# Kernel optimization log

Measured on AMD Instinct MI355X. Metric: run time of the kernel, lower is better.

Reference implementation:

```python
import jax, jax.numpy as jnp
import numpy as np

B, X_DIM, Y_DIM, HIDDEN = 512, 768, 128, 1024
H2 = HIDDEN // 2


def setup_inputs() -> dict:
    key = jax.random.key(0)
    ks = jax.random.split(key, 10)
    s_in = 1.0 / np.sqrt(X_DIM)
    s_h = 1.0 / np.sqrt(H2)
    return {
        "x_samples": jax.random.normal(ks[0], (B, X_DIM), jnp.float32),
        "y_samples": jax.random.normal(ks[1], (B, Y_DIM), jnp.float32),
        "w1_mu": jax.random.uniform(ks[2], (X_DIM, H2), jnp.float32, -s_in, s_in),
        "b1_mu": jax.random.uniform(ks[3], (H2,), jnp.float32, -s_in, s_in),
        "w2_mu": jax.random.uniform(ks[4], (H2, Y_DIM), jnp.float32, -s_h, s_h),
        "b2_mu": jax.random.uniform(ks[5], (Y_DIM,), jnp.float32, -s_h, s_h),
        "w1_lv": jax.random.uniform(ks[6], (X_DIM, H2), jnp.float32, -s_in, s_in),
        "b1_lv": jax.random.uniform(ks[7], (H2,), jnp.float32, -s_in, s_in),
        "w2_lv": jax.random.uniform(ks[8], (H2, Y_DIM), jnp.float32, -s_h, s_h),
        "b2_lv": jax.random.uniform(ks[9], (Y_DIM,), jnp.float32, -s_h, s_h),
    }


def reference(x_samples, y_samples, w1_mu, b1_mu, w2_mu, b2_mu,
              w1_lv, b1_lv, w2_lv, b2_lv):
    batch = y_samples.shape[0]
    # p_mu / p_logvar MLP heads
    mu = jax.nn.relu(x_samples @ w1_mu + b1_mu) @ w2_mu + b2_mu          # [B, Y]
    logvar = jnp.tanh(jax.nn.relu(x_samples @ w1_lv + b1_lv) @ w2_lv + b2_lv)  # [B, Y]

    inv_var = jnp.exp(-logvar)
    # positive: diagonal Gaussian log-prob of y_i under p(.|x_i), up to const
    positive = (-0.5 * (mu - y_samples) ** 2 * inv_var - 0.5 * logvar).sum(-1)  # [B]

    # pairwise log-probs: row i = params from x_i, col j = sample y_j
    mu_1 = mu[:, None, :]            # [B, 1, Y]
    lv_1 = logvar[:, None, :]        # [B, 1, Y]
    y_1 = y_samples[None, :, :]      # [1, B, Y]
    all_probs = (-0.5 * (y_1 - mu_1) ** 2 * jnp.exp(-lv_1) - 0.5 * lv_1).sum(-1)  # [B, B]

    # Faithful replication of the torch broadcasting: diag_mask is [B, B, 1],
    # so all_probs + diag_mask broadcasts to [B, B, B], then logsumexp over dim 0.
    diag_mask = (jnp.eye(batch, dtype=all_probs.dtype) * -20.0)[:, :, None]  # [B, B, 1]
    logits = all_probs + diag_mask                                           # [B, B, B]
    negative = jax.scipy.special.logsumexp(logits, axis=0) - jnp.log(batch - 1.0)  # [B, B]

    return (positive - negative).mean()
```

## Files before the change

### kernel.cpp

```cpp
#include <hip/hip_runtime.h>
#include <math.h>

#define BSZ   512
#define XD    768
#define YD    128
#define H2D   512

__global__ __launch_bounds__(256, 2) void layer1_kernel(
    const float* __restrict__ x,
    const float* __restrict__ w1_mu, const float* __restrict__ w1_lv,
    const float* __restrict__ y,
    float* __restrict__ p1,
    double* __restrict__ Sy, double* __restrict__ Sy2,
    double* __restrict__ accum, unsigned int* __restrict__ counter)
{
    __shared__ float As[16][68];
    __shared__ float Bs[16][68];
    const int t = threadIdx.x;

    if (blockIdx.z == 4) {
        const int id = blockIdx.x + 8 * blockIdx.y;
        if (id >= 16) return;
        const int dl = t & 7;
        const int g  = t >> 3;
        const int d  = id * 8 + dl;
        float s = 0.f, s2 = 0.f;
        for (int i = g * 16; i < g * 16 + 16; ++i) {
            const float v = y[i * YD + d];
            s += v; s2 += v * v;
        }
        float* shs  = &As[0][0];
        float* shs2 = &Bs[0][0];
        shs[t] = s; shs2[t] = s2;
        __syncthreads();
        if (t < 8) {
            double S = 0.0, S2 = 0.0;
            #pragma unroll
            for (int gg = 0; gg < 32; ++gg) {
                S += (double)shs[gg * 8 + t]; S2 += (double)shs2[gg * 8 + t];
            }
            Sy[id * 8 + t] = S; Sy2[id * 8 + t] = S2;
        } else if (id == 0 && t == 8)  { accum[0] = 0.0; }
        else if (id == 0 && t == 9)  { accum[1] = 0.0; }
        else if (id == 0 && t == 10) { *counter = 0u; }
        return;
    }

    const int bz     = blockIdx.z;
    const int branch = bz >> 1;
    const int ks     = bz & 1;
    const float* __restrict__ W = branch ? w1_lv : w1_mu;
    float* __restrict__ out = p1 + (size_t)bz * (BSZ * H2D);

    const int m0 = blockIdx.x * 64;
    const int n0 = blockIdx.y * 64;
    const int tx = t & 15;
    const int ty = t >> 4;

    const int am  = t >> 2;
    const int akq = (t & 3) << 2;
    const int bkk = t >> 4;
    const int bnq = (t & 15) << 2;

    const int kbase = ks * 384;
    float acc[4][4] = {};

    float4 a_pref = *(const float4*)&x[(m0 + am) * XD + kbase + akq];
    float4 b_pref = *(const float4*)&W[(kbase + bkk) * H2D + n0 + bnq];

    for (int kt = 0; kt < 384; kt += 16) {
        __syncthreads();
        As[akq + 0][am] = a_pref.x;
        As[akq + 1][am] = a_pref.y;
        As[akq + 2][am] = a_pref.z;
        As[akq + 3][am] = a_pref.w;
        *(float4*)&Bs[bkk][bnq] = b_pref;
        __syncthreads();
        if (kt + 16 < 384) {
            const int kn = kbase + kt + 16;
            a_pref = *(const float4*)&x[(m0 + am) * XD + kn + akq];
            b_pref = *(const float4*)&W[(kn + bkk) * H2D + n0 + bnq];
        }
        #pragma unroll
        for (int k = 0; k < 16; ++k) {
            const float4 av = *(const float4*)&As[k][ty * 4];
            const float4 bv = *(const float4*)&Bs[k][tx * 4];
            acc[0][0] += av.x*bv.x; acc[0][1] += av.x*bv.y; acc[0][2] += av.x*bv.z; acc[0][3] += av.x*bv.w;
            acc[1][0] += av.y*bv.x; acc[1][1] += av.y*bv.y; acc[1][2] += av.y*bv.z; acc[1][3] += av.y*bv.w;
            acc[2][0] += av.z*bv.x; acc[2][1] += av.z*bv.y; acc[2][2] += av.z*bv.z; acc[2][3] += av.z*bv.w;
            acc[3][0] += av.w*bv.x; acc[3][1] += av.w*bv.y; acc[3][2] += av.w*bv.z; acc[3][3] += av.w*bv.w;
        }
    }

    #pragma unroll
    for (int i = 0; i < 4; ++i) {
        const float4 o = make_float4(acc[i][0], acc[i][1], acc[i][2], acc[i][3]);
        *(float4*)&out[(m0 + ty * 4 + i) * H2D + n0 + tx * 4] = o;
    }
}

__global__ __launch_bounds__(256, 2) void layer2_kernel(
    const float* __restrict__ p1,
    const float* __restrict__ b1_mu, const float* __restrict__ b1_lv,
    const float* __restrict__ w2_mu, const float* __restrict__ w2_lv,
    float* __restrict__ p2)
{
    __shared__ float As[16][68];
    __shared__ float Bs[16][68];
    const int t = threadIdx.x;

    const int branch = blockIdx.z >> 3;
    const int ks     = blockIdx.z & 7;
    const float* __restrict__ pa = p1 + (size_t)(branch * 2 + 0) * (BSZ * H2D);
    const float* __restrict__ pb = p1 + (size_t)(branch * 2 + 1) * (BSZ * H2D);
    const float* __restrict__ b1 = branch ? b1_lv : b1_mu;
    const float* __restrict__ W  = branch ? w2_lv : w2_mu;
    float* __restrict__ out = p2 + (size_t)blockIdx.z * (BSZ * YD);

    const int m0 = blockIdx.x * 64;
    const int n0 = blockIdx.y * 64;
    const int tx = t & 15;
    const int ty = t >> 4;

    const int am  = t >> 2;
    const int akq = (t & 3) << 2;
    const int bkk = t >> 4;
    const int bnq = (t & 15) << 2;

    const int kbase = ks * 64;
    float acc[4][4] = {};

    float4 pa4 = *(const float4*)&pa[(m0 + am) * H2D + kbase + akq];
    float4 pb4 = *(const float4*)&pb[(m0 + am) * H2D + kbase + akq];
    float4 bb4 = *(const float4*)&b1[kbase + akq];
    float4 w4  = *(const float4*)&W[(kbase + bkk) * YD + n0 + bnq];

    for (int kt = 0; kt < 64; kt += 16) {
        __syncthreads();
        As[akq + 0][am] = fmaxf(pa4.x + pb4.x + bb4.x, 0.f);
        As[akq + 1][am] = fmaxf(pa4.y + pb4.y + bb4.y, 0.f);
        As[akq + 2][am] = fmaxf(pa4.z + pb4.z + bb4.z, 0.f);
        As[akq + 3][am] = fmaxf(pa4.w + pb4.w + bb4.w, 0.f);
        *(float4*)&Bs[bkk][bnq] = w4;
        __syncthreads();
        if (kt + 16 < 64) {
            const int kn = kbase + kt + 16;
            pa4 = *(const float4*)&pa[(m0 + am) * H2D + kn + akq];
            pb4 = *(const float4*)&pb[(m0 + am) * H2D + kn + akq];
            bb4 = *(const float4*)&b1[kn + akq];
            w4  = *(const float4*)&W[(kn + bkk) * YD + n0 + bnq];
        }
        #pragma unroll
        for (int k = 0; k < 16; ++k) {
            const float4 av = *(const float4*)&As[k][ty * 4];
            const float4 bv = *(const float4*)&Bs[k][tx * 4];
            acc[0][0] += av.x*bv.x; acc[0][1] += av.x*bv.y; acc[0][2] += av.x*bv.z; acc[0][3] += av.x*bv.w;
            acc[1][0] += av.y*bv.x; acc[1][1] += av.y*bv.y; acc[1][2] += av.y*bv.z; acc[1][3] += av.y*bv.w;
            acc[2][0] += av.z*bv.x; acc[2][1] += av.z*bv.y; acc[2][2] += av.z*bv.z; acc[2][3] += av.z*bv.w;
            acc[3][0] += av.w*bv.x; acc[3][1] += av.w*bv.y; acc[3][2] += av.w*bv.z; acc[3][3] += av.w*bv.w;
        }
    }

    #pragma unroll
    for (int i = 0; i < 4; ++i) {
        const float4 o = make_float4(acc[i][0], acc[i][1], acc[i][2], acc[i][3]);
        *(float4*)&out[(m0 + ty * 4 + i) * YD + n0 + tx * 4] = o;
    }
}

__global__ __launch_bounds__(256) void reduce_kernel(
    const float* __restrict__ p2, const float* __restrict__ y,
    const float* __restrict__ b2_mu, const float* __restrict__ b2_lv,
    const double* __restrict__ Sy, const double* __restrict__ Sy2,
    double* __restrict__ accum, unsigned int* __restrict__ counter,
    float* __restrict__ outp)
{
    const int NE = BSZ * YD;
    const int e  = blockIdx.x * 256 + threadIdx.x;
    const int d  = e & (YD - 1);

    float mu = b2_mu[d];
    float lp = b2_lv[d];
    #pragma unroll
    for (int s = 0; s < 8; ++s) {
        mu += p2[s * NE + e];
        lp += p2[(8 + s) * NE + e];
    }
    const float lv = tanhf(lp);
    const float iv = expf(-lv);
    const float dm = mu - y[e];

    double pos = -0.5 * (double)dm * (double)dm * (double)iv - 0.5 * (double)lv;
    double ap  = (double)iv * (-0.5 * Sy2[d] + (double)mu * Sy[d]
                               - 256.0 * (double)mu * (double)mu)
               - 256.0 * (double)lv;

    #pragma unroll
    for (int off = 32; off > 0; off >>= 1) {
        pos += __shfl_down(pos, off);
        ap  += __shfl_down(ap, off);
    }
    __shared__ double sp[4];
    __shared__ double sa[4];
    const int lane = threadIdx.x & 63;
    const int wv   = threadIdx.x >> 6;
    if (lane == 0) { sp[wv] = pos; sa[wv] = ap; }
    __syncthreads();
    if (threadIdx.x == 0) {
        atomicAdd(&accum[0], sp[0] + sp[1] + sp[2] + sp[3]);
        atomicAdd(&accum[1], sa[0] + sa[1] + sa[2] + sa[3]);
        __threadfence();
        const unsigned int old = atomicAdd(counter, 1u);
        if (old == 255u) {
            const double P = atomicAdd(&accum[0], 0.0);
            const double A = atomicAdd(&accum[1], 0.0);
            const double C = log1p(exp(-20.0) / 511.0);
            outp[0] = (float)(P / 512.0 - A / 262144.0 - C);
        }
    }
}

extern "C" void kernel_launch(void* const* d_in, const int* in_sizes, int n_in,
                              void* d_out, int out_size, void* d_ws, size_t ws_size,
                              hipStream_t stream) {
    const float* x     = (const float*)d_in[0];
    const float* y     = (const float*)d_in[1];
    const float* w1_mu = (const float*)d_in[2];
    const float* b1_mu = (const float*)d_in[3];
    const float* w2_mu = (const float*)d_in[4];
    const float* b2_mu = (const float*)d_in[5];
    const float* w1_lv = (const float*)d_in[6];
    const float* b1_lv = (const float*)d_in[7];
    const float* w2_lv = (const float*)d_in[8];
    const float* b2_lv = (const float*)d_in[9];

    char* ws = (char*)d_ws;
    float*  p1 = (float*)(ws);
    float*  p2 = (float*)(ws + (size_t)4 * BSZ * H2D * 4);
    double* Sy = (double*)(ws + (size_t)4 * BSZ * H2D * 4
                              + (size_t)16 * BSZ * YD * 4);
    double* Sy2 = Sy + YD;
    double* accum = Sy2 + YD;
    unsigned int* counter = (unsigned int*)(accum + 2);

    layer1_kernel<<<dim3(8, 8, 5), 256, 0, stream>>>(
        x, w1_mu, w1_lv, y, p1, Sy, Sy2, accum, counter);
    layer2_kernel<<<dim3(8, 2, 16), 256, 0, stream>>>(
        p1, b1_mu, b1_lv, w2_mu, w2_lv, p2);
    reduce_kernel<<<256, 256, 0, stream>>>(
        p2, y, b2_mu, b2_lv, Sy, Sy2, accum, counter, (float*)d_out);
}
```

Before: 109.6 us.

## Retile layer1 GEMM to 128x64 with 4-way split-K and separate y-sum kernel

Layer 1 now uses 128x64 output tiles with 8 rows per thread and splits K four ways instead of two, giving 256 GEMM blocks. The y column-sum work moves into its own small kernel, and layer 2 sums four partial products plus the bias before the ReLU. The aim is more register reuse per shared-memory load and better CU occupancy on the layer-1 GEMM. The cost is twice the p1 workspace traffic, more partial loads in layer 2, and one extra kernel launch.

```diff
diff --git a/kernel.cpp b/kernel.cpp
--- a/kernel.cpp
+++ b/kernel.cpp
@@ -6,51 +6,125 @@
 #define YD    128
 #define H2D   512
 
-__global__ __launch_bounds__(256, 2) void layer1_kernel(
+__global__ __launch_bounds__(256) void ysum_kernel(
+    const float* __restrict__ y, double* __restrict__ Sy,
+    double* __restrict__ Sy2, double* __restrict__ accum,
+    unsigned int* __restrict__ counter)
+{
+    const int t  = threadIdx.x;
+    const int dl = t & 3;
+    const int g  = t >> 2;
+    const int d  = blockIdx.x * 4 + dl;
+
+    float s = 0.f, s2 = 0.f;
+    #pragma unroll
+    for (int i = g * 8; i < g * 8 + 8; ++i) {
+        const float v = y[i * YD + d];
+        s += v; s2 += v * v;
+    }
+    __shared__ float sh[256];
+    __shared__ float sh2[256];
+    sh[g * 4 + dl] = s; sh2[g * 4 + dl] = s2;
+    __syncthreads();
+    if (t < 4) {
+        double S = 0.0, S2 = 0.0;
+        #pragma unroll
+        for (int gg = 0; gg < 64; ++gg) {
+            S += (double)sh[gg * 4 + t]; S2 += (double)sh2[gg * 4 + t];
+        }
+        Sy[blockIdx.x * 4 + t] = S; Sy2[blockIdx.x * 4 + t] = S2;
+    } else if (blockIdx.x == 0 && t == 4) { accum[0] = 0.0; }
+    else if (blockIdx.x == 0 && t == 5) { accum[1] = 0.0; }
+    else if (blockIdx.x == 0 && t == 6) { *counter = 0u; }
+}
+
+__global__ __launch_bounds__(256) void layer1_kernel(
     const float* __restrict__ x,
     const float* __restrict__ w1_mu, const float* __restrict__ w1_lv,
-    const float* __restrict__ y,
-    float* __restrict__ p1,
-    double* __restrict__ Sy, double* __restrict__ Sy2,
-    double* __restrict__ accum, unsigned int* __restrict__ counter)
+    float* __restrict__ p1)
+{
+    __shared__ float As[16][132];
+    __shared__ float Bs[16][68];
+
+    const int t      = threadIdx.x;
+    const int branch = blockIdx.z >> 2;
+    const int ks     = blockIdx.z & 3;
+    const float* __restrict__ W = branch ? w1_lv : w1_mu;
+    float* __restrict__ out = p1 + (size_t)blockIdx.z * (BSZ * H2D);
+
+    const int m0 = blockIdx.x * 128;
+    const int n0 = blockIdx.y * 64;
+    const int tx = t & 15;
+    const int ty = t >> 4;
+
+    const int am  = t >> 1;
+    const int akq = (t & 1) * 8;
+    const int bkk = t >> 4;
+    const int bnq = (t & 15) * 4;
+
+    const int kbase = ks * 192;
+    float acc[8][4] = {};
+
+    float4 a_p0 = *(const float4*)&x[(m0 + am) * XD + kbase + akq];
+    float4 a_p1 = *(const float4*)&x[(m0 + am) * XD + kbase + akq + 4];
+    float4 b_p  = *(const float4*)&W[(kbase + bkk) * H2D + n0 + bnq];
+
+    for (int kt = 0; kt < 192; kt += 16) {
+        __syncthreads();
+        As[akq + 0][am] = a_p0.x; As[akq + 1][am] = a_p0.y;
+        As[akq + 2][am] = a_p0.z; As[akq + 3][am] = a_p0.w;
+        As[akq + 4][am] = a_p1.x; As[akq + 5][am] = a_p1.y;
+        As[akq + 6][am] = a_p1.z; As[akq + 7][am] = a_p1.w;
+        *(float4*)&Bs[bkk][bnq] = b_p;
+        __syncthreads();
+        if (kt + 16 < 192) {
+            const int kn = kbase + kt + 16;
+            a_p0 = *(const float4*)&x[(m0 + am) * XD + kn + akq];
+            a_p1 = *(const float4*)&x[(m0 + am) * XD + kn + akq + 4];
+            b_p  = *(const float4*)&W[(kn + bkk) * H2D + n0 + bnq];
+        }
+        #pragma unroll
+        for (int k = 0; k < 16; ++k) {
+            const float4 a0 = *(const float4*)&As[k][ty * 8];
+            const float4 a1 = *(const float4*)&As[k][ty * 8 + 4];
+            const float4 bv = *(const float4*)&Bs[k][tx * 4];
+            acc[0][0] += a0.x*bv.x; acc[0][1] += a0.x*bv.y; acc[0][2] += a0.x*bv.z; acc[0][3] += a0.x*bv.w;
+            acc[1][0] += a0.y*bv.x; acc[1][1] += a0.y*bv.y; acc[1][2] += a0.y*bv.z; acc[1][3] += a0.y*bv.w;
+            acc[2][0] += a0.z*bv.x; acc[2][1] += a0.z*bv.y; acc[2][2] += a0.z*bv.z; acc[2][3] += a0.z*bv.w;
+            acc[3][0] += a0.w*bv.x; acc[3][1] += a0.w*bv.y; acc[3][2] += a0.w*bv.z; acc[3][3] += a0.w*bv.w;
+            acc[4][0] += a1.x*bv.x; acc[4][1] += a1.x*bv.y; acc[4][2] += a1.x*bv.z; acc[4][3] += a1.x*bv.w;
+            acc[5][0] += a1.y*bv.x; acc[5][1] += a1.y*bv.y; acc[5][2] += a1.y*bv.z; acc[5][3] += a1.y*bv.w;
+            acc[6][0] += a1.z*bv.x; acc[6][1] += a1.z*bv.y; acc[6][2] += a1.z*bv.z; acc[6][3] += a1.z*bv.w;
+            acc[7][0] += a1.w*bv.x; acc[7][1] += a1.w*bv.y; acc[7][2] += a1.w*bv.z; acc[7][3] += a1.w*bv.w;
+        }
+    }
+
+    #pragma unroll
+    for (int i = 0; i < 8; ++i) {
+        const float4 o = make_float4(acc[i][0], acc[i][1], acc[i][2], acc[i][3]);
+        *(float4*)&out[(m0 + ty * 8 + i) * H2D + n0 + tx * 4] = o;
+    }
+}
+
+__global__ __launch_bounds__(256) void layer2_kernel(
+    const float* __restrict__ p1,
+    const float* __restrict__ b1_mu, const float* __restrict__ b1_lv,
+    const float* __restrict__ w2_mu, const float* __restrict__ w2_lv,
+    float* __restrict__ p2)
 {
     __shared__ float As[16][68];
     __shared__ float Bs[16][68];
-    const int t = threadIdx.x;
-
-    if (blockIdx.z == 4) {
-        const int id = blockIdx.x + 8 * blockIdx.y;
-        if (id >= 16) return;
-        const int dl = t & 7;
-        const int g  = t >> 3;
-        const int d  = id * 8 + dl;
-        float s = 0.f, s2 = 0.f;
-        for (int i = g * 16; i < g * 16 + 16; ++i) {
-            const float v = y[i * YD + d];
-            s += v; s2 += v * v;
-        }
-        float* shs  = &As[0][0];
-        float* shs2 = &Bs[0][0];
-        shs[t] = s; shs2[t] = s2;
-        __syncthreads();
-        if (t < 8) {
-            double S = 0.0, S2 = 0.0;
-            #pragma unroll
-            for (int gg = 0; gg < 32; ++gg) {
-                S += (double)shs[gg * 8 + t]; S2 += (double)shs2[gg * 8 + t];
-            }
-            Sy[id * 8 + t] = S; Sy2[id * 8 + t] = S2;
-        } else if (id == 0 && t == 8)  { accum[0] = 0.0; }
-        else if (id == 0 && t == 9)  { accum[1] = 0.0; }
-        else if (id == 0 && t == 10) { *counter = 0u; }
-        return;
-    }
-
-    const int bz     = blockIdx.z;
-    const int branch = bz >> 1;
-    const int ks     = bz & 1;
-    const float* __restrict__ W = branch ? w1_lv : w1_mu;
-    float* __restrict__ out = p1 + (size_t)bz * (BSZ * H2D);
+
+    const int t      = threadIdx.x;
+    const int branch = blockIdx.z >> 3;
+    const int ks     = blockIdx.z & 7;
+    const float* __restrict__ q0 = p1 + (size_t)(branch * 4 + 0) * (BSZ * H2D);
+    const float* __restrict__ q1 = p1 + (size_t)(branch * 4 + 1) * (BSZ * H2D);
+    const float* __restrict__ q2 = p1 + (size_t)(branch * 4 + 2) * (BSZ * H2D);
+    const float* __restrict__ q3 = p1 + (size_t)(branch * 4 + 3) * (BSZ * H2D);
+    const float* __restrict__ b1 = branch ? b1_lv : b1_mu;
+    const float* __restrict__ W  = branch ? w2_lv : w2_mu;
+    float* __restrict__ out = p2 + (size_t)blockIdx.z * (BSZ * YD);
 
     const int m0 = blockIdx.x * 64;
     const int n0 = blockIdx.y * 64;
@@ -58,97 +132,37 @@
     const int ty = t >> 4;
 
     const int am  = t >> 2;
-    const int akq = (t & 3) << 2;
+    const int akq = (t & 3) * 4;
     const int bkk = t >> 4;
-    const int bnq = (t & 15) << 2;
-
-    const int kbase = ks * 384;
-    float acc[4][4] = {};
-
-    float4 a_pref = *(const float4*)&x[(m0 + am) * XD + kbase + akq];
-    float4 b_pref = *(const float4*)&W[(kbase + bkk) * H2D + n0 + bnq];
-
-    for (int kt = 0; kt < 384; kt += 16) {
-        __syncthreads();
-        As[akq + 0][am] = a_pref.x;
-        As[akq + 1][am] = a_pref.y;
-        As[akq + 2][am] = a_pref.z;
-        As[akq + 3][am] = a_pref.w;
-        *(float4*)&Bs[bkk][bnq] = b_pref;
-        __syncthreads();
-        if (kt + 16 < 384) {
-            const int kn = kbase + kt + 16;
-            a_pref = *(const float4*)&x[(m0 + am) * XD + kn + akq];
-            b_pref = *(const float4*)&W[(kn + bkk) * H2D + n0 + bnq];
-        }
-        #pragma unroll
-        for (int k = 0; k < 16; ++k) {
-            const float4 av = *(const float4*)&As[k][ty * 4];
-            const float4 bv = *(const float4*)&Bs[k][tx * 4];
-            acc[0][0] += av.x*bv.x; acc[0][1] += av.x*bv.y; acc[0][2] += av.x*bv.z; acc[0][3] += av.x*bv.w;
-            acc[1][0] += av.y*bv.x; acc[1][1] += av.y*bv.y; acc[1][2] += av.y*bv.z; acc[1][3] += av.y*bv.w;
-            acc[2][0] += av.z*bv.x; acc[2][1] += av.z*bv.y; acc[2][2] += av.z*bv.z; acc[2][3] += av.z*bv.w;
-            acc[3][0] += av.w*bv.x; acc[3][1] += av.w*bv.y; acc[3][2] += av.w*bv.z; acc[3][3] += av.w*bv.w;
-        }
-    }
-
-    #pragma unroll
-    for (int i = 0; i < 4; ++i) {
-        const float4 o = make_float4(acc[i][0], acc[i][1], acc[i][2], acc[i][3]);
-        *(float4*)&out[(m0 + ty * 4 + i) * H2D + n0 + tx * 4] = o;
-    }
-}
-
-__global__ __launch_bounds__(256, 2) void layer2_kernel(
-    const float* __restrict__ p1,
-    const float* __restrict__ b1_mu, const float* __restrict__ b1_lv,
-    const float* __restrict__ w2_mu, const float* __restrict__ w2_lv,
-    float* __restrict__ p2)
-{
-    __shared__ float As[16][68];
-    __shared__ float Bs[16][68];
-    const int t = threadIdx.x;
-
-    const int branch = blockIdx.z >> 3;
-    const int ks     = blockIdx.z & 7;
-    const float* __restrict__ pa = p1 + (size_t)(branch * 2 + 0) * (BSZ * H2D);
-    const float* __restrict__ pb = p1 + (size_t)(branch * 2 + 1) * (BSZ * H2D);
-    const float* __restrict__ b1 = branch ? b1_lv : b1_mu;
-    const float* __restrict__ W  = branch ? w2_lv : w2_mu;
-    float* __restrict__ out = p2 + (size_t)blockIdx.z * (BSZ * YD);
-
-    const int m0 = blockIdx.x * 64;
-    const int n0 = blockIdx.y * 64;
-    const int tx = t & 15;
-    const int ty = t >> 4;
-
-    const int am  = t >> 2;
-    const int akq = (t & 3) << 2;
-    const int bkk = t >> 4;
-    const int bnq = (t & 15) << 2;
+    const int bnq = (t & 15) * 4;
 
     const int kbase = ks * 64;
     float acc[4][4] = {};
 
-    float4 pa4 = *(const float4*)&pa[(m0 + am) * H2D + kbase + akq];
-    float4 pb4 = *(const float4*)&pb[(m0 + am) * H2D + kbase + akq];
-    float4 bb4 = *(const float4*)&b1[kbase + akq];
-    float4 w4  = *(const float4*)&W[(kbase + bkk) * YD + n0 + bnq];
+    const int arow = (m0 + am) * H2D;
+    float4 s0 = *(const float4*)&q0[arow + kbase + akq];
+    float4 s1 = *(const float4*)&q1[arow + kbase + akq];
+    float4 s2 = *(const float4*)&q2[arow + kbase + akq];
+    float4 s3 = *(const float4*)&q3[arow + kbase + akq];
+    float4 bb = *(const float4*)&b1[kbase + akq];
+    float4 w4 = *(const float4*)&W[(kbase + bkk) * YD + n0 + bnq];
 
     for (int kt = 0; kt < 64; kt += 16) {
         __syncthreads();
-        As[akq + 0][am] = fmaxf(pa4.x + pb4.x + bb4.x, 0.f);
-        As[akq + 1][am] = fmaxf(pa4.y + pb4.y + bb4.y, 0.f);
-        As[akq + 2][am] = fmaxf(pa4.z + pb4.z + bb4.z, 0.f);
-        As[akq + 3][am] = fmaxf(pa4.w + pb4.w + bb4.w, 0.f);
+        As[akq + 0][am] = fmaxf(s0.x + s1.x + s2.x + s3.x + bb.x, 0.f);
+        As[akq + 1][am] = fmaxf(s0.y + s1.y + s2.y + s3.y + bb.y, 0.f);
+        As[akq + 2][am] = fmaxf(s0.z + s1.z + s2.z + s3.z + bb.z, 0.f);
+        As[akq + 3][am] = fmaxf(s0.w + s1.w + s2.w + s3.w + bb.w, 0.f);
         *(float4*)&Bs[bkk][bnq] = w4;
         __syncthreads();
         if (kt + 16 < 64) {
             const int kn = kbase + kt + 16;
-            pa4 = *(const float4*)&pa[(m0 + am) * H2D + kn + akq];
-            pb4 = *(const float4*)&pb[(m0 + am) * H2D + kn + akq];
-            bb4 = *(const float4*)&b1[kn + akq];
-            w4  = *(const float4*)&W[(kn + bkk) * YD + n0 + bnq];
+            s0 = *(const float4*)&q0[arow + kn + akq];
+            s1 = *(const float4*)&q1[arow + kn + akq];
+            s2 = *(const float4*)&q2[arow + kn + akq];
+            s3 = *(const float4*)&q3[arow + kn + akq];
+            bb = *(const float4*)&b1[kn + akq];
+            w4 = *(const float4*)&W[(kn + bkk) * YD + n0 + bnq];
         }
         #pragma unroll
         for (int k = 0; k < 16; ++k) {
@@ -236,15 +250,15 @@
 
     char* ws = (char*)d_ws;
     float*  p1 = (float*)(ws);
-    float*  p2 = (float*)(ws + (size_t)4 * BSZ * H2D * 4);
-    double* Sy = (double*)(ws + (size_t)4 * BSZ * H2D * 4
+    float*  p2 = (float*)(ws + (size_t)8 * BSZ * H2D * 4);
+    double* Sy = (double*)(ws + (size_t)8 * BSZ * H2D * 4
                               + (size_t)16 * BSZ * YD * 4);
     double* Sy2 = Sy + YD;
     double* accum = Sy2 + YD;
     unsigned int* counter = (unsigned int*)(accum + 2);
 
-    layer1_kernel<<<dim3(8, 8, 5), 256, 0, stream>>>(
-        x, w1_mu, w1_lv, y, p1, Sy, Sy2, accum, counter);
+    ysum_kernel<<<32, 256, 0, stream>>>(y, Sy, Sy2, accum, counter);
+    layer1_kernel<<<dim3(4, 8, 8), 256, 0, stream>>>(x, w1_mu, w1_lv, p1);
     layer2_kernel<<<dim3(8, 2, 16), 256, 0, stream>>>(
         p1, b1_mu, b1_lv, w2_mu, w2_lv, p2);
     reduce_kernel<<<256, 256, 0, stream>>>(
```

New measurement: 114.0 us. 1.04x slower.

## Rebalance GEMM split-K and tiling across both layers, move y-stats to layer2

Applied to the files above, without the earlier changes.

Layer1 now splits K eightfold with 128x64 tiles (8x4 per thread) instead of twofold with 64x64 tiles. That gives 512 blocks instead of 256, to fill more CUs and do more work per thread. Layer2 sums the eight partials on load and uses 32x128 tiles with 16-way split-K, and it absorbs the y statistics work. The cost is more partial-sum traffic through workspace: 16 layer1 partial buffers and 32 layer2 partial buffers are written and read back.

```diff
diff --git a/kernel.cpp b/kernel.cpp
--- a/kernel.cpp
+++ b/kernel.cpp
@@ -9,22 +9,91 @@
 __global__ __launch_bounds__(256, 2) void layer1_kernel(
     const float* __restrict__ x,
     const float* __restrict__ w1_mu, const float* __restrict__ w1_lv,
+    float* __restrict__ p1)
+{
+    __shared__ float As[16][132];
+    __shared__ float Bs[16][68];
+
+    const int t      = threadIdx.x;
+    const int branch = blockIdx.z >> 3;
+    const int ks     = blockIdx.z & 7;
+    const float* __restrict__ W = branch ? w1_lv : w1_mu;
+    float* __restrict__ out = p1 + (size_t)blockIdx.z * (BSZ * H2D);
+
+    const int m0 = blockIdx.x * 128;
+    const int n0 = blockIdx.y * 64;
+    const int tx = t & 15;
+    const int ty = t >> 4;
+
+    const int am  = t >> 1;
+    const int akq = (t & 1) * 8;
+    const int bkk = t >> 4;
+    const int bnq = (t & 15) * 4;
+
+    const int kbase = ks * 96;
+    float acc[8][4] = {};
+
+    float4 a0p = *(const float4*)&x[(m0 + am) * XD + kbase + akq];
+    float4 a1p = *(const float4*)&x[(m0 + am) * XD + kbase + akq + 4];
+    float4 bp  = *(const float4*)&W[(kbase + bkk) * H2D + n0 + bnq];
+
+    for (int kt = 0; kt < 96; kt += 16) {
+        __syncthreads();
+        As[akq + 0][am] = a0p.x; As[akq + 1][am] = a0p.y;
+        As[akq + 2][am] = a0p.z; As[akq + 3][am] = a0p.w;
+        As[akq + 4][am] = a1p.x; As[akq + 5][am] = a1p.y;
+        As[akq + 6][am] = a1p.z; As[akq + 7][am] = a1p.w;
+        *(float4*)&Bs[bkk][bnq] = bp;
+        __syncthreads();
+        if (kt + 16 < 96) {
+            const int kn = kbase + kt + 16;
+            a0p = *(const float4*)&x[(m0 + am) * XD + kn + akq];
+            a1p = *(const float4*)&x[(m0 + am) * XD + kn + akq + 4];
+            bp  = *(const float4*)&W[(kn + bkk) * H2D + n0 + bnq];
+        }
+        #pragma unroll
+        for (int k = 0; k < 16; ++k) {
+            const float4 a0 = *(const float4*)&As[k][ty * 8];
+            const float4 a1 = *(const float4*)&As[k][ty * 8 + 4];
+            const float4 bv = *(const float4*)&Bs[k][tx * 4];
+            acc[0][0] += a0.x*bv.x; acc[0][1] += a0.x*bv.y; acc[0][2] += a0.x*bv.z; acc[0][3] += a0.x*bv.w;
+            acc[1][0] += a0.y*bv.x; acc[1][1] += a0.y*bv.y; acc[1][2] += a0.y*bv.z; acc[1][3] += a0.y*bv.w;
+            acc[2][0] += a0.z*bv.x; acc[2][1] += a0.z*bv.y; acc[2][2] += a0.z*bv.z; acc[2][3] += a0.z*bv.w;
+            acc[3][0] += a0.w*bv.x; acc[3][1] += a0.w*bv.y; acc[3][2] += a0.w*bv.z; acc[3][3] += a0.w*bv.w;
+            acc[4][0] += a1.x*bv.x; acc[4][1] += a1.x*bv.y; acc[4][2] += a1.x*bv.z; acc[4][3] += a1.x*bv.w;
+            acc[5][0] += a1.y*bv.x; acc[5][1] += a1.y*bv.y; acc[5][2] += a1.y*bv.z; acc[5][3] += a1.y*bv.w;
+            acc[6][0] += a1.z*bv.x; acc[6][1] += a1.z*bv.y; acc[6][2] += a1.z*bv.z; acc[6][3] += a1.z*bv.w;
+            acc[7][0] += a1.w*bv.x; acc[7][1] += a1.w*bv.y; acc[7][2] += a1.w*bv.z; acc[7][3] += a1.w*bv.w;
+        }
+    }
+
+    #pragma unroll
+    for (int i = 0; i < 8; ++i) {
+        const float4 o = make_float4(acc[i][0], acc[i][1], acc[i][2], acc[i][3]);
+        *(float4*)&out[(m0 + ty * 8 + i) * H2D + n0 + tx * 4] = o;
+    }
+}
+
+__global__ __launch_bounds__(256, 2) void layer2_kernel(
+    const float* __restrict__ p1,
+    const float* __restrict__ b1_mu, const float* __restrict__ b1_lv,
+    const float* __restrict__ w2_mu, const float* __restrict__ w2_lv,
     const float* __restrict__ y,
-    float* __restrict__ p1,
+    float* __restrict__ p2,
     double* __restrict__ Sy, double* __restrict__ Sy2,
     double* __restrict__ accum, unsigned int* __restrict__ counter)
 {
-    __shared__ float As[16][68];
-    __shared__ float Bs[16][68];
+    __shared__ float As[16][36];
+    __shared__ float Bs[16][132];
     const int t = threadIdx.x;
 
-    if (blockIdx.z == 4) {
-        const int id = blockIdx.x + 8 * blockIdx.y;
-        if (id >= 16) return;
+    if (blockIdx.z == 32) {
+        const int id = blockIdx.x;
         const int dl = t & 7;
         const int g  = t >> 3;
         const int d  = id * 8 + dl;
         float s = 0.f, s2 = 0.f;
+        #pragma unroll
         for (int i = g * 16; i < g * 16 + 16; ++i) {
             const float v = y[i * YD + d];
             s += v; s2 += v * v;
@@ -46,125 +115,85 @@
         return;
     }
 
-    const int bz     = blockIdx.z;
-    const int branch = bz >> 1;
-    const int ks     = bz & 1;
-    const float* __restrict__ W = branch ? w1_lv : w1_mu;
-    float* __restrict__ out = p1 + (size_t)bz * (BSZ * H2D);
-
-    const int m0 = blockIdx.x * 64;
-    const int n0 = blockIdx.y * 64;
-    const int tx = t & 15;
-    const int ty = t >> 4;
-
-    const int am  = t >> 2;
-    const int akq = (t & 3) << 2;
-    const int bkk = t >> 4;
-    const int bnq = (t & 15) << 2;
-
-    const int kbase = ks * 384;
-    float acc[4][4] = {};
-
-    float4 a_pref = *(const float4*)&x[(m0 + am) * XD + kbase + akq];
-    float4 b_pref = *(const float4*)&W[(kbase + bkk) * H2D + n0 + bnq];
-
-    for (int kt = 0; kt < 384; kt += 16) {
-        __syncthreads();
-        As[akq + 0][am] = a_pref.x;
-        As[akq + 1][am] = a_pref.y;
-        As[akq + 2][am] = a_pref.z;
-        As[akq + 3][am] = a_pref.w;
-        *(float4*)&Bs[bkk][bnq] = b_pref;
-        __syncthreads();
-        if (kt + 16 < 384) {
-            const int kn = kbase + kt + 16;
-            a_pref = *(const float4*)&x[(m0 + am) * XD + kn + akq];
-            b_pref = *(const float4*)&W[(kn + bkk) * H2D + n0 + bnq];
-        }
-        #pragma unroll
-        for (int k = 0; k < 16; ++k) {
-            const float4 av = *(const float4*)&As[k][ty * 4];
-            const float4 bv = *(const float4*)&Bs[k][tx * 4];
-            acc[0][0] += av.x*bv.x; acc[0][1] += av.x*bv.y; acc[0][2] += av.x*bv.z; acc[0][3] += av.x*bv.w;
-            acc[1][0] += av.y*bv.x; acc[1][1] += av.y*bv.y; acc[1][2] += av.y*bv.z; acc[1][3] += av.y*bv.w;
-            acc[2][0] += av.z*bv.x; acc[2][1] += av.z*bv.y; acc[2][2] += av.z*bv.z; acc[2][3] += av.z*bv.w;
-            acc[3][0] += av.w*bv.x; acc[3][1] += av.w*bv.y; acc[3][2] += av.w*bv.z; acc[3][3] += av.w*bv.w;
-        }
-    }
-
-    #pragma unroll
-    for (int i = 0; i < 4; ++i) {
-        const float4 o = make_float4(acc[i][0], acc[i][1], acc[i][2], acc[i][3]);
-        *(float4*)&out[(m0 + ty * 4 + i) * H2D + n0 + tx * 4] = o;
-    }
-}
-
-__global__ __launch_bounds__(256, 2) void layer2_kernel(
-    const float* __restrict__ p1,
-    const float* __restrict__ b1_mu, const float* __restrict__ b1_lv,
-    const float* __restrict__ w2_mu, const float* __restrict__ w2_lv,
-    float* __restrict__ p2)
-{
-    __shared__ float As[16][68];
-    __shared__ float Bs[16][68];
-    const int t = threadIdx.x;
-
-    const int branch = blockIdx.z >> 3;
-    const int ks     = blockIdx.z & 7;
-    const float* __restrict__ pa = p1 + (size_t)(branch * 2 + 0) * (BSZ * H2D);
-    const float* __restrict__ pb = p1 + (size_t)(branch * 2 + 1) * (BSZ * H2D);
+    const int branch = blockIdx.z >> 4;
+    const int ks2    = blockIdx.z & 15;
+    const float* __restrict__ q  = p1 + (size_t)(branch * 8) * (BSZ * H2D);
     const float* __restrict__ b1 = branch ? b1_lv : b1_mu;
     const float* __restrict__ W  = branch ? w2_lv : w2_mu;
     float* __restrict__ out = p2 + (size_t)blockIdx.z * (BSZ * YD);
 
-    const int m0 = blockIdx.x * 64;
-    const int n0 = blockIdx.y * 64;
+    const int m0 = blockIdx.x * 32;
     const int tx = t & 15;
     const int ty = t >> 4;
 
     const int am  = t >> 2;
-    const int akq = (t & 3) << 2;
+    const int akq = (t & 3) * 4;
     const int bkk = t >> 4;
-    const int bnq = (t & 15) << 2;
-
-    const int kbase = ks * 64;
-    float acc[4][4] = {};
-
-    float4 pa4 = *(const float4*)&pa[(m0 + am) * H2D + kbase + akq];
-    float4 pb4 = *(const float4*)&pb[(m0 + am) * H2D + kbase + akq];
-    float4 bb4 = *(const float4*)&b1[kbase + akq];
-    float4 w4  = *(const float4*)&W[(kbase + bkk) * YD + n0 + bnq];
-
-    for (int kt = 0; kt < 64; kt += 16) {
-        __syncthreads();
-        As[akq + 0][am] = fmaxf(pa4.x + pb4.x + bb4.x, 0.f);
-        As[akq + 1][am] = fmaxf(pa4.y + pb4.y + bb4.y, 0.f);
-        As[akq + 2][am] = fmaxf(pa4.z + pb4.z + bb4.z, 0.f);
-        As[akq + 3][am] = fmaxf(pa4.w + pb4.w + bb4.w, 0.f);
-        *(float4*)&Bs[bkk][bnq] = w4;
-        __syncthreads();
-        if (kt + 16 < 64) {
-            const int kn = kbase + kt + 16;
-            pa4 = *(const float4*)&pa[(m0 + am) * H2D + kn + akq];
-            pb4 = *(const float4*)&pb[(m0 + am) * H2D + kn + akq];
-            bb4 = *(const float4*)&b1[kn + akq];
-            w4  = *(const float4*)&W[(kn + bkk) * YD + n0 + bnq];
+    const int bnq = (t & 15) * 8;
+
+    const int kbase = ks2 * 32;
+    float acc[2][2][4] = {};
+
+    float4 aval, bb4;
+    if (t < 128) {
+        const int arow = (m0 + am) * H2D + kbase + akq;
+        aval = *(const float4*)&q[arow];
+        #pragma unroll
+        for (int s = 1; s < 8; ++s) {
+            const float4 v = *(const float4*)&q[(size_t)s * (BSZ * H2D) + arow];
+            aval.x += v.x; aval.y += v.y; aval.z += v.z; aval.w += v.w;
+        }
+        bb4 = *(const float4*)&b1[kbase + akq];
+    }
+    float4 w0 = *(const float4*)&W[(kbase + bkk) * YD + bnq];
+    float4 w1 = *(const float4*)&W[(kbase + bkk) * YD + bnq + 4];
+
+    for (int kt = 0; kt < 32; kt += 16) {
+        __syncthreads();
+        if (t < 128) {
+            As[akq + 0][am] = fmaxf(aval.x + bb4.x, 0.f);
+            As[akq + 1][am] = fmaxf(aval.y + bb4.y, 0.f);
+            As[akq + 2][am] = fmaxf(aval.z + bb4.z, 0.f);
+            As[akq + 3][am] = fmaxf(aval.w + bb4.w, 0.f);
+        }
+        *(float4*)&Bs[bkk][bnq]     = w0;
+        *(float4*)&Bs[bkk][bnq + 4] = w1;
+        __syncthreads();
+        if (kt == 0) {
+            const int kn = kbase + 16;
+            if (t < 128) {
+                const int arow = (m0 + am) * H2D + kn + akq;
+                aval = *(const float4*)&q[arow];
+                #pragma unroll
+                for (int s = 1; s < 8; ++s) {
+                    const float4 v = *(const float4*)&q[(size_t)s * (BSZ * H2D) + arow];
+                    aval.x += v.x; aval.y += v.y; aval.z += v.z; aval.w += v.w;
+                }
+                bb4 = *(const float4*)&b1[kn + akq];
+            }
+            w0 = *(const float4*)&W[(kn + bkk) * YD + bnq];
+            w1 = *(const float4*)&W[(kn + bkk) * YD + bnq + 4];
         }
         #pragma unroll
         for (int k = 0; k < 16; ++k) {
-            const float4 av = *(const float4*)&As[k][ty * 4];
-            const float4 bv = *(const float4*)&Bs[k][tx * 4];
-            acc[0][0] += av.x*bv.x; acc[0][1] += av.x*bv.y; acc[0][2] += av.x*bv.z; acc[0][3] += av.x*bv.w;
-            acc[1][0] += av.y*bv.x; acc[1][1] += av.y*bv.y; acc[1][2] += av.y*bv.z; acc[1][3] += av.y*bv.w;
-            acc[2][0] += av.z*bv.x; acc[2][1] += av.z*bv.y; acc[2][2] += av.z*bv.z; acc[2][3] += av.z*bv.w;
-            acc[3][0] += av.w*bv.x; acc[3][1] += av.w*bv.y; acc[3][2] += av.w*bv.z; acc[3][3] += av.w*bv.w;
-        }
-    }
-
-    #pragma unroll
-    for (int i = 0; i < 4; ++i) {
-        const float4 o = make_float4(acc[i][0], acc[i][1], acc[i][2], acc[i][3]);
-        *(float4*)&out[(m0 + ty * 4 + i) * YD + n0 + tx * 4] = o;
+            const float a0 = As[k][ty * 2 + 0];
+            const float a1 = As[k][ty * 2 + 1];
+            const float4 v0 = *(const float4*)&Bs[k][tx * 4];
+            const float4 v1 = *(const float4*)&Bs[k][64 + tx * 4];
+            acc[0][0][0] += a0*v0.x; acc[0][0][1] += a0*v0.y; acc[0][0][2] += a0*v0.z; acc[0][0][3] += a0*v0.w;
+            acc[0][1][0] += a0*v1.x; acc[0][1][1] += a0*v1.y; acc[0][1][2] += a0*v1.z; acc[0][1][3] += a0*v1.w;
+            acc[1][0][0] += a1*v0.x; acc[1][0][1] += a1*v0.y; acc[1][0][2] += a1*v0.z; acc[1][0][3] += a1*v0.w;
+            acc[1][1][0] += a1*v1.x; acc[1][1][1] += a1*v1.y; acc[1][1][2] += a1*v1.z; acc[1][1][3] += a1*v1.w;
+        }
+    }
+
+    #pragma unroll
+    for (int r = 0; r < 2; ++r) {
+        const int row = (m0 + ty * 2 + r) * YD;
+        float4 o0 = make_float4(acc[r][0][0], acc[r][0][1], acc[r][0][2], acc[r][0][3]);
+        float4 o1 = make_float4(acc[r][1][0], acc[r][1][1], acc[r][1][2], acc[r][1][3]);
+        *(float4*)&out[row + tx * 4]      = o0;
+        *(float4*)&out[row + 64 + tx * 4] = o1;
     }
 }
 
@@ -182,9 +211,9 @@
     float mu = b2_mu[d];
     float lp = b2_lv[d];
     #pragma unroll
-    for (int s = 0; s < 8; ++s) {
+    for (int s = 0; s < 16; ++s) {
         mu += p2[s * NE + e];
-        lp += p2[(8 + s) * NE + e];
+        lp += p2[(16 + s) * NE + e];
     }
     const float lv = tanhf(lp);
     const float iv = expf(-lv);
@@ -236,17 +265,16 @@
 
     char* ws = (char*)d_ws;
     float*  p1 = (float*)(ws);
-    float*  p2 = (float*)(ws + (size_t)4 * BSZ * H2D * 4);
-    double* Sy = (double*)(ws + (size_t)4 * BSZ * H2D * 4
-                              + (size_t)16 * BSZ * YD * 4);
+    float*  p2 = (float*)(ws + (size_t)16 * BSZ * H2D * 4);
+    double* Sy = (double*)(ws + (size_t)16 * BSZ * H2D * 4
+                              + (size_t)32 * BSZ * YD * 4);
     double* Sy2 = Sy + YD;
     double* accum = Sy2 + YD;
     unsigned int* counter = (unsigned int*)(accum + 2);
 
-    layer1_kernel<<<dim3(8, 8, 5), 256, 0, stream>>>(
-        x, w1_mu, w1_lv, y, p1, Sy, Sy2, accum, counter);
-    layer2_kernel<<<dim3(8, 2, 16), 256, 0, stream>>>(
-        p1, b1_mu, b1_lv, w2_mu, w2_lv, p2);
+    layer1_kernel<<<dim3(4, 8, 16), 256, 0, stream>>>(x, w1_mu, w1_lv, p1);
+    layer2_kernel<<<dim3(16, 1, 33), 256, 0, stream>>>(
+        p1, b1_mu, b1_lv, w2_mu, w2_lv, y, p2, Sy, Sy2, accum, counter);
     reduce_kernel<<<256, 256, 0, stream>>>(
         p2, y, b2_mu, b2_lv, Sy, Sy2, accum, counter, (float*)d_out);
 }
```

New measurement: 112.3 us. +2.4%, slower.
